# Performance work log

Hardware: AMD Instinct MI355X
Metric: run time of the kernel (lower is better)

The kernel has to match this reference:

```python
import jax, jax.numpy as jnp
import numpy as np

B, SQ, SKV, D = 4, 2048, 2048, 1024
HEADS, DIM_HEAD = 16, 64
SCALE = DIM_HEAD ** -0.5


def setup_inputs() -> dict:
    key = jax.random.key(0)
    ks = jax.random.split(key, 7)
    s = 0.02  # keep pre-softmax logits in a sane range
    return {
        "hidden_states": jax.random.normal(ks[0], (B, SQ, D), dtype=jnp.float32),
        "encoder_hidden_states": jax.random.normal(ks[1], (B, SKV, D), dtype=jnp.float32),
        "Wq": jax.random.normal(ks[2], (D, D), dtype=jnp.float32) * s,
        "Wk": jax.random.normal(ks[3], (D, D), dtype=jnp.float32) * s,
        "Wv": jax.random.normal(ks[4], (D, D), dtype=jnp.float32) * s,
        "Wo": jax.random.normal(ks[5], (D, D), dtype=jnp.float32) * s,
        "bo": jnp.zeros((D,), dtype=jnp.float32),
    }


def reference(hidden_states, encoder_hidden_states, Wq, Wk, Wv, Wo, bo):
    # to_q / to_k / to_v (bias=False)
    q = hidden_states @ Wq                       # [B, SQ, H*Dh]
    k = encoder_hidden_states @ Wk               # [B, SKV, H*Dh]
    v = encoder_hidden_states @ Wv
    # head split: [B, S, H, Dh]
    q = q.reshape(B, SQ, HEADS, DIM_HEAD)
    k = k.reshape(B, SKV, HEADS, DIM_HEAD)
    v = v.reshape(B, SKV, HEADS, DIM_HEAD)
    # scaled QK^T (baddbmm with beta=0, alpha=scale), softmax over keys
    scores = jnp.einsum("bqhd,bkhd->bhqk", q, k) * SCALE  # [B, H, SQ, SKV]
    probs = jax.nn.softmax(scores, axis=-1)
    # attention-weighted values, merge heads
    out = jnp.einsum("bhqk,bkhd->bqhd", probs, v).reshape(B, SQ, HEADS * DIM_HEAD)
    # to_out[0] linear (with bias); to_out[1] Dropout(0.0) is identity
    return out @ Wo + bo
```

## Files before the change

kernel.cpp:

```cpp
#include <hip/hip_runtime.h>

#define BATCH 4
#define SQ 2048
#define SKV 2048
#define DMODEL 1024
#define HEADS 16
#define DH 64

typedef __bf16 bf8_t __attribute__((ext_vector_type(8)));
typedef float f4_t __attribute__((ext_vector_type(4)));
typedef float f16_t __attribute__((ext_vector_type(16)));
typedef unsigned int u32;
typedef unsigned short ush;

static __device__ __forceinline__ ush f2bf(float f) {
  __bf16 h = (__bf16)f;
  return __builtin_bit_cast(ush, h);
}
static __device__ __forceinline__ u32 pk2(float a, float b) {
  return (u32)f2bf(a) | ((u32)f2bf(b) << 16);
}
static __device__ __forceinline__ void async16(const ush* g, ush* l) {
  __builtin_amdgcn_global_load_lds((const __attribute__((address_space(1))) unsigned int*)g,
                                   (__attribute__((address_space(3))) unsigned int*)l, 16, 0, 0);
}
static __device__ __forceinline__ void barrier_f() {
  asm volatile("" ::: "memory");
  __builtin_amdgcn_s_barrier();
  asm volatile("" ::: "memory");
}

__global__ __launch_bounds__(256) void prep_k(const float* __restrict__ hs,
                                              const float* __restrict__ ehs,
                                              const float* __restrict__ W0,
                                              const float* __restrict__ W1,
                                              const float* __restrict__ W2,
                                              const float* __restrict__ W3,
                                              ush* __restrict__ wT,
                                              ush* __restrict__ hsb, ush* __restrict__ ehsb) {
  __shared__ ush t[64][72];
  const int bx = blockIdx.x;
  const int tid = threadIdx.x;
  if (bx < 8192) {
    const float* X = bx < 4096 ? hs : ehs;
    ush* Y = bx < 4096 ? hsb : ehsb;
    const size_t i = ((size_t)(bx & 4095) * 256 + tid) * 8;
    float4 a = *reinterpret_cast<const float4*>(X + i);
    float4 b = *reinterpret_cast<const float4*>(X + i + 4);
    uint4 u = {pk2(a.x, a.y), pk2(a.z, a.w), pk2(b.x, b.y), pk2(b.z, b.w)};
    *reinterpret_cast<uint4*>(Y + i) = u;
    return;
  }
  const int idx = bx - 8192;
  const int z = idx >> 8, kb = (idx >> 4) & 15, nb = idx & 15;
  const float* W = z == 0 ? W0 : z == 1 ? W1 : z == 2 ? W2 : W3;
  const float scl = (z == 0) ? 0.125f * 1.44269504088896f : 1.0f;
  ush* o = wT + (size_t)z * (DMODEL * DMODEL);
  const int k0 = kb * 64, n0 = nb * 64;
#pragma unroll
  for (int it = 0; it < 4; ++it) {
    int c = tid + it * 256;
    int r = c >> 4, q4 = c & 15;
    float4 v = *reinterpret_cast<const float4*>(&W[(size_t)(k0 + r) * DMODEL + n0 + q4 * 4]);
    t[q4 * 4 + 0][r] = f2bf(v.x * scl);
    t[q4 * 4 + 1][r] = f2bf(v.y * scl);
    t[q4 * 4 + 2][r] = f2bf(v.z * scl);
    t[q4 * 4 + 3][r] = f2bf(v.w * scl);
  }
  __syncthreads();
#pragma unroll
  for (int it = 0; it < 2; ++it) {
    int c = tid + it * 256;
    int r = c >> 3, s8 = c & 7;
    uint4 pv;
    pv.x = (u32)t[r][s8 * 8 + 0] | ((u32)t[r][s8 * 8 + 1] << 16);
    pv.y = (u32)t[r][s8 * 8 + 2] | ((u32)t[r][s8 * 8 + 3] << 16);
    pv.z = (u32)t[r][s8 * 8 + 4] | ((u32)t[r][s8 * 8 + 5] << 16);
    pv.w = (u32)t[r][s8 * 8 + 6] | ((u32)t[r][s8 * 8 + 7] << 16);
    *reinterpret_cast<uint4*>(&o[(size_t)(n0 + r) * DMODEL + k0 + s8 * 8]) = pv;
  }
}

__global__ __launch_bounds__(256, 2) void proj_k(const ush* __restrict__ hsb,
                                                 const ush* __restrict__ ehsb,
                                                 const ush* __restrict__ AO,
                                                 const ush* __restrict__ wT,
                                                 ush* __restrict__ Qb, ush* __restrict__ K2,
                                                 ush* __restrict__ V2, float* __restrict__ out,
                                                 const float* __restrict__ bias, int segbase) {
  __shared__ ush As[2][128 * 64];
  __shared__ ush Bs[2][128 * 64];
  const int tid = threadIdx.x;
  const int lane = tid & 63, w = tid >> 6;
  const int wr = w >> 1, wc = w & 1;
  const int lr = lane & 15, lg = lane >> 4;
  const int bid = blockIdx.x;
  const int seg = segbase + (bid >> 9);
  const int t = bid & 511;
  const int m0 = (t >> 3) * 128, n0 = (t & 7) * 128;
  const ush* A = seg == 0 ? hsb : (seg == 3 ? AO : ehsb);
  const ush* BT = wT + (size_t)seg * (DMODEL * DMODEL);

  auto stage = [&](int bf, int kt) {
    const int kb = kt * 64;
#pragma unroll
    for (int ch = 0; ch < 4; ++ch) {
      const int g = ch * 256 + tid;
      const int r = g >> 3, s8 = (g & 7) ^ (r & 7);
      async16(A + (size_t)(m0 + r) * DMODEL + kb + s8 * 8, &As[bf][(ch * 256 + w * 64) * 8]);
      async16(BT + (size_t)(n0 + r) * DMODEL + kb + s8 * 8, &Bs[bf][(ch * 256 + w * 64) * 8]);
    }
  };

  f4_t acc[4][4] = {};
  stage(0, 0);
  for (int kt = 0; kt < DMODEL / 64; ++kt) {
    const int cur = kt & 1;
    barrier_f();
    if (kt + 1 < DMODEL / 64) {
      stage(cur ^ 1, kt + 1);
      asm volatile("s_waitcnt vmcnt(8)" ::: "memory");
    } else {
      asm volatile("s_waitcnt vmcnt(0)" ::: "memory");
    }
    barrier_f();
#pragma unroll
    for (int ks = 0; ks < 2; ++ks) {
      bf8_t a[4], b[4];
#pragma unroll
      for (int rf = 0; rf < 4; ++rf) {
        const int row = wr * 64 + rf * 16 + lr;
        a[rf] = *reinterpret_cast<const bf8_t*>(
            &As[cur][(row * 64 + ks * 32 + lg * 8) ^ ((row & 7) << 3)]);
      }
#pragma unroll
      for (int cf = 0; cf < 4; ++cf) {
        const int nn = wc * 64 + cf * 16 + lr;
        b[cf] = *reinterpret_cast<const bf8_t*>(
            &Bs[cur][(nn * 64 + ks * 32 + lg * 8) ^ ((nn & 7) << 3)]);
      }
      __builtin_amdgcn_s_setprio(1);
#pragma unroll
      for (int rf = 0; rf < 4; ++rf)
#pragma unroll
        for (int cf = 0; cf < 4; ++cf)
          acc[rf][cf] = __builtin_amdgcn_mfma_f32_16x16x32_bf16(a[rf], b[cf], acc[rf][cf], 0, 0, 0);
      __builtin_amdgcn_s_setprio(0);
    }
  }
  if (seg == 1 || seg == 2) {
    ush* L = &As[0][0];
    barrier_f();
#pragma unroll
    for (int rf = 0; rf < 4; ++rf)
#pragma unroll
      for (int cf = 0; cf < 4; ++cf) {
        const int nl = wc * 64 + cf * 16 + lr;
        const int h2 = nl >> 6, dd = nl & 63;
#pragma unroll
        for (int i = 0; i < 4; ++i) {
          const int kvl = wr * 64 + rf * 16 + lg * 4 + i;
          const int kt2 = kvl >> 6, s = kvl & 63;
          int idx;
          if (seg == 1) {
            idx = ((h2 * 2 + kt2) << 12) + (((dd >> 4) * 2 + ((dd >> 3) & 1)) << 9) +
                  (s << 3) + (dd & 7);
          } else {
            idx = ((h2 * 2 + kt2) << 12) + (((s >> 4) * 2 + ((s >> 3) & 1)) << 9) +
                  (dd << 3) + (s & 7);
          }
          L[idx] = f2bf(acc[rf][cf][i]);
        }
      }
    barrier_f();
    ush* G = (seg == 1) ? K2 : V2;
    const int bb = m0 >> 11, kt0 = (m0 & 2047) >> 6;
    const int h0 = n0 >> 6;
#pragma unroll
    for (int j = 0; j < 4; ++j) {
      const size_t dst =
          ((size_t)(bb * 16 + h0 + (j >> 1)) * 32 + kt0 + (j & 1)) * 4096 + tid * 16;
      *reinterpret_cast<uint4*>(&G[dst]) =
          *reinterpret_cast<const uint4*>(&L[j * 4096 + tid * 16]);
      *reinterpret_cast<uint4*>(&G[dst + 8]) =
          *reinterpret_cast<const uint4*>(&L[j * 4096 + tid * 16 + 8]);
    }
  } else if (seg == 3) {
#pragma unroll
    for (int cf = 0; cf < 4; ++cf) {
      const int col = n0 + wc * 64 + cf * 16 + lr;
      const float bv = bias[col];
#pragma unroll
      for (int rf = 0; rf < 4; ++rf)
#pragma unroll
        for (int i = 0; i < 4; ++i) {
          const int row = m0 + wr * 64 + rf * 16 + lg * 4 + i;
          out[(size_t)row * DMODEL + col] = acc[rf][cf][i] + bv;
        }
    }
  } else {
#pragma unroll
    for (int rf = 0; rf < 4; ++rf)
#pragma unroll
      for (int cf = 0; cf < 4; ++cf)
#pragma unroll
        for (int i = 0; i < 4; ++i) {
          const int row = m0 + wr * 64 + rf * 16 + lg * 4 + i;
          const int col = n0 + wc * 64 + cf * 16 + lr;
          Qb[(size_t)row * DMODEL + col] = f2bf(acc[rf][cf][i]);
        }
  }
}

__global__ __launch_bounds__(256, 4) void attn_k(const ush* __restrict__ Qb,
                                                 const ush* __restrict__ K2,
                                                 const ush* __restrict__ V2,
                                                 ush* __restrict__ AO) {
  __shared__ ush Ks[2][4096];
  __shared__ ush Vs[2][4096];
  const int tid = threadIdx.x;
  const int lane = tid & 63, w = tid >> 6;
  const int rw = lane & 31, hi = lane >> 5;

  const int bid = blockIdx.x;
  const int swz = (bid & 7) * 128 + (bid >> 3);
  const int hl = swz >> 4;
  const int qb = swz & 15;
  const int b = hl >> 4, h = hl & 15;
  const int q0 = qb * 128 + w * 32;

  const ush* Qp = Qb + ((size_t)(b * SQ + q0 + rw)) * DMODEL + h * DH + hi * 8;
  bf8_t qf[4];
#pragma unroll
  for (int f = 0; f < 4; ++f) qf[f] = *reinterpret_cast<const bf8_t*>(Qp + 16 * f);

  bf8_t ones;
#pragma unroll
  for (int i = 0; i < 8; ++i) ones[i] = __builtin_bit_cast(__bf16, (ush)0x3F80);

  f16_t acc0 = {}, acc1 = {}, sacc = {};

  const ush* Kh = K2 + (size_t)hl * 131072;
  const ush* Vh = V2 + (size_t)hl * 131072;

  auto stage = [&](int bf, int kt) {
    const ush* ksrc = Kh + (size_t)kt * 4096;
    const ush* vsrc = Vh + (size_t)kt * 4096;
#pragma unroll
    for (int ch = 0; ch < 2; ++ch) {
      const int off = (ch * 256 + tid) * 8;
      async16(ksrc + off, &Ks[bf][(ch * 256 + w * 64) * 8]);
      async16(vsrc + off, &Vs[bf][(ch * 256 + w * 64) * 8]);
    }
  };

  stage(0, 0);
  int cur = 0;
  for (int kt = 0; kt < SKV / 64; ++kt) {
    barrier_f();
    if (kt + 1 < SKV / 64) {
      stage(cur ^ 1, kt + 1);
      asm volatile("s_waitcnt vmcnt(4)" ::: "memory");
    } else {
      asm volatile("s_waitcnt vmcnt(0)" ::: "memory");
    }
    barrier_f();

    f16_t s0 = {}, s1 = {};
    __builtin_amdgcn_s_setprio(1);
#pragma unroll
    for (int f = 0; f < 4; ++f) {
      const int base = (f * 128 + hi * 64 + rw) * 8;
      bf8_t k0 = *reinterpret_cast<const bf8_t*>(&Ks[cur][base]);
      bf8_t k1 = *reinterpret_cast<const bf8_t*>(&Ks[cur][base + 256]);
      s0 = __builtin_amdgcn_mfma_f32_32x32x16_bf16(k0, qf[f], s0, 0, 0, 0);
      s1 = __builtin_amdgcn_mfma_f32_32x32x16_bf16(k1, qf[f], s1, 0, 0, 0);
    }
    __builtin_amdgcn_s_setprio(0);

#pragma unroll
    for (int i = 0; i < 16; ++i) s0[i] = __builtin_amdgcn_exp2f(s0[i]);
#pragma unroll
    for (int i = 0; i < 16; ++i) s1[i] = __builtin_amdgcn_exp2f(s1[i]);

    __builtin_amdgcn_s_setprio(1);
#pragma unroll
    for (int kb = 0; kb < 2; ++kb) {
      const f16_t& sv = kb ? s1 : s0;
      bf8_t pf[2];
      {
        u32 w0 = pk2(sv[0], sv[1]), w2 = pk2(sv[4], sv[5]);
        asm volatile("v_permlane32_swap_b32 %0, %1" : "+v"(w0), "+v"(w2));
        u32 w1 = pk2(sv[2], sv[3]), w3 = pk2(sv[6], sv[7]);
        asm volatile("v_permlane32_swap_b32 %0, %1" : "+v"(w1), "+v"(w3));
        uint4 t0 = {w0, w1, w2, w3};
        pf[0] = __builtin_bit_cast(bf8_t, t0);
        u32 x0 = pk2(sv[8], sv[9]), x2 = pk2(sv[12], sv[13]);
        asm volatile("v_permlane32_swap_b32 %0, %1" : "+v"(x0), "+v"(x2));
        u32 x1 = pk2(sv[10], sv[11]), x3 = pk2(sv[14], sv[15]);
        asm volatile("v_permlane32_swap_b32 %0, %1" : "+v"(x1), "+v"(x3));
        uint4 t1 = {x0, x1, x2, x3};
        pf[1] = __builtin_bit_cast(bf8_t, t1);
      }
#pragma unroll
      for (int s = 0; s < 2; ++s) {
        const int vbase = ((2 * kb + s) * 128 + hi * 64 + rw) * 8;
        bf8_t v0 = *reinterpret_cast<const bf8_t*>(&Vs[cur][vbase]);
        bf8_t v1 = *reinterpret_cast<const bf8_t*>(&Vs[cur][vbase + 256]);
        acc0 = __builtin_amdgcn_mfma_f32_32x32x16_bf16(v0, pf[s], acc0, 0, 0, 0);
        acc1 = __builtin_amdgcn_mfma_f32_32x32x16_bf16(v1, pf[s], acc1, 0, 0, 0);
        sacc = __builtin_amdgcn_mfma_f32_32x32x16_bf16(ones, pf[s], sacc, 0, 0, 0);
      }
    }
    __builtin_amdgcn_s_setprio(0);
    cur ^= 1;
  }

  const float inv = 1.f / sacc[0];
  ush* Op = AO + ((size_t)(b * SQ + q0 + rw)) * DMODEL + h * DH;
#pragma unroll
  for (int db = 0; db < 2; ++db) {
    const f16_t& A = db ? acc1 : acc0;
#pragma unroll
    for (int r = 0; r < 16; r += 2) {
      const int d = db * 32 + (r & 3) + 8 * (r >> 2) + 4 * hi;
      *reinterpret_cast<u32*>(Op + d) = pk2(A[r] * inv, A[r + 1] * inv);
    }
  }
}

extern "C" void kernel_launch(void* const* d_in, const int* in_sizes, int n_in,
                              void* d_out, int out_size, void* d_ws, size_t ws_size,
                              hipStream_t stream) {
  const float* hs = (const float*)d_in[0];
  const float* ehs = (const float*)d_in[1];
  const float* Wq = (const float*)d_in[2];
  const float* Wk = (const float*)d_in[3];
  const float* Wv = (const float*)d_in[4];
  const float* Wo = (const float*)d_in[5];
  const float* bo = (const float*)d_in[6];
  float* out = (float*)d_out;

  unsigned short* ws = (unsigned short*)d_ws;
  const size_t MM = (size_t)1024 * 1024;
  unsigned short* wT = ws;
  unsigned short* Qb = ws + 4 * MM;
  unsigned short* K2 = Qb + 8 * MM;
  unsigned short* V2 = K2 + 8 * MM;
  unsigned short* AO = V2 + 8 * MM;
  unsigned short* hsb = (unsigned short*)d_out;
  unsigned short* ehsb = hsb + 8 * MM;

  prep_k<<<dim3(9216), 256, 0, stream>>>(hs, ehs, Wq, Wk, Wv, Wo, wT, hsb, ehsb);
  proj_k<<<dim3(1536), 256, 0, stream>>>(hsb, ehsb, AO, wT, Qb, K2, V2, out, bo, 0);
  attn_k<<<dim3(1024), 256, 0, stream>>>(Qb, K2, V2, AO);
  proj_k<<<dim3(512), 256, 0, stream>>>(hsb, ehsb, AO, wT, Qb, K2, V2, out, bo, 3);
}
```

Baseline: 207.3 us.

## Load K/V fragments directly from global memory and sum probabilities with VALU

The attention kernel drops the LDS double-buffered K/V staging and its barriers; each wave now loads its K and V MFMA fragments straight from global memory into registers every tile. The row-sum of exponentials is computed with VALU adds plus a cross-half shuffle instead of an extra MFMA against a ones vector. Occupancy hint drops from 4 to 3 blocks per CU because of higher register use. The cost is that every wave in a block re-reads the same K/V tiles from global/L2 instead of sharing them through LDS, and load latency is no longer hidden by explicit prefetch.

```diff
diff --git a/kernel.cpp b/kernel.cpp
--- a/kernel.cpp
+++ b/kernel.cpp
@@ -212,12 +212,10 @@
   }
 }
 
-__global__ __launch_bounds__(256, 4) void attn_k(const ush* __restrict__ Qb,
+__global__ __launch_bounds__(256, 3) void attn_k(const ush* __restrict__ Qb,
                                                  const ush* __restrict__ K2,
                                                  const ush* __restrict__ V2,
                                                  ush* __restrict__ AO) {
-  __shared__ ush Ks[2][4096];
-  __shared__ ush Vs[2][4096];
   const int tid = threadIdx.x;
   const int lane = tid & 63, w = tid >> 6;
   const int rw = lane & 31, hi = lane >> 5;
@@ -234,47 +232,36 @@
 #pragma unroll
   for (int f = 0; f < 4; ++f) qf[f] = *reinterpret_cast<const bf8_t*>(Qp + 16 * f);
 
-  bf8_t ones;
-#pragma unroll
-  for (int i = 0; i < 8; ++i) ones[i] = __builtin_bit_cast(__bf16, (ush)0x3F80);
-
-  f16_t acc0 = {}, acc1 = {}, sacc = {};
-
-  const ush* Kh = K2 + (size_t)hl * 131072;
-  const ush* Vh = V2 + (size_t)hl * 131072;
-
-  auto stage = [&](int bf, int kt) {
-    const ush* ksrc = Kh + (size_t)kt * 4096;
-    const ush* vsrc = Vh + (size_t)kt * 4096;
-#pragma unroll
-    for (int ch = 0; ch < 2; ++ch) {
-      const int off = (ch * 256 + tid) * 8;
-      async16(ksrc + off, &Ks[bf][(ch * 256 + w * 64) * 8]);
-      async16(vsrc + off, &Vs[bf][(ch * 256 + w * 64) * 8]);
-    }
-  };
-
-  stage(0, 0);
-  int cur = 0;
+  f16_t acc0 = {}, acc1 = {};
+  float lsum = 0.f;
+
+  const int fo = (hi * 64 + rw) * 8;
+  const ush* Kh = K2 + (size_t)hl * 131072 + fo;
+  const ush* Vh = V2 + (size_t)hl * 131072 + fo;
+
   for (int kt = 0; kt < SKV / 64; ++kt) {
-    barrier_f();
-    if (kt + 1 < SKV / 64) {
-      stage(cur ^ 1, kt + 1);
-      asm volatile("s_waitcnt vmcnt(4)" ::: "memory");
-    } else {
-      asm volatile("s_waitcnt vmcnt(0)" ::: "memory");
-    }
-    barrier_f();
+    const ush* kp = Kh + kt * 4096;
+    const ush* vp = Vh + kt * 4096;
+
+    bf8_t kf0[4], kf1[4];
+#pragma unroll
+    for (int f = 0; f < 4; ++f) {
+      kf0[f] = *reinterpret_cast<const bf8_t*>(kp + f * 1024);
+      kf1[f] = *reinterpret_cast<const bf8_t*>(kp + f * 1024 + 256);
+    }
+    bf8_t vf0[4], vf1[4];
+#pragma unroll
+    for (int g = 0; g < 4; ++g) {
+      vf0[g] = *reinterpret_cast<const bf8_t*>(vp + g * 1024);
+      vf1[g] = *reinterpret_cast<const bf8_t*>(vp + g * 1024 + 256);
+    }
 
     f16_t s0 = {}, s1 = {};
     __builtin_amdgcn_s_setprio(1);
 #pragma unroll
     for (int f = 0; f < 4; ++f) {
-      const int base = (f * 128 + hi * 64 + rw) * 8;
-      bf8_t k0 = *reinterpret_cast<const bf8_t*>(&Ks[cur][base]);
-      bf8_t k1 = *reinterpret_cast<const bf8_t*>(&Ks[cur][base + 256]);
-      s0 = __builtin_amdgcn_mfma_f32_32x32x16_bf16(k0, qf[f], s0, 0, 0, 0);
-      s1 = __builtin_amdgcn_mfma_f32_32x32x16_bf16(k1, qf[f], s1, 0, 0, 0);
+      s0 = __builtin_amdgcn_mfma_f32_32x32x16_bf16(kf0[f], qf[f], s0, 0, 0, 0);
+      s1 = __builtin_amdgcn_mfma_f32_32x32x16_bf16(kf1[f], qf[f], s1, 0, 0, 0);
     }
     __builtin_amdgcn_s_setprio(0);
 
@@ -282,6 +269,21 @@
     for (int i = 0; i < 16; ++i) s0[i] = __builtin_amdgcn_exp2f(s0[i]);
 #pragma unroll
     for (int i = 0; i < 16; ++i) s1[i] = __builtin_amdgcn_exp2f(s1[i]);
+    {
+      float t0 = 0.f, t1 = 0.f, t2 = 0.f, t3 = 0.f;
+#pragma unroll
+      for (int i = 0; i < 16; i += 4) {
+        t0 += s0[i];
+        t1 += s0[i + 1];
+        t2 += s0[i + 2];
+        t3 += s0[i + 3];
+        t0 += s1[i];
+        t1 += s1[i + 1];
+        t2 += s1[i + 2];
+        t3 += s1[i + 3];
+      }
+      lsum += (t0 + t1) + (t2 + t3);
+    }
 
     __builtin_amdgcn_s_setprio(1);
 #pragma unroll
@@ -304,19 +306,16 @@
       }
 #pragma unroll
       for (int s = 0; s < 2; ++s) {
-        const int vbase = ((2 * kb + s) * 128 + hi * 64 + rw) * 8;
-        bf8_t v0 = *reinterpret_cast<const bf8_t*>(&Vs[cur][vbase]);
-        bf8_t v1 = *reinterpret_cast<const bf8_t*>(&Vs[cur][vbase + 256]);
-        acc0 = __builtin_amdgcn_mfma_f32_32x32x16_bf16(v0, pf[s], acc0, 0, 0, 0);
-        acc1 = __builtin_amdgcn_mfma_f32_32x32x16_bf16(v1, pf[s], acc1, 0, 0, 0);
-        sacc = __builtin_amdgcn_mfma_f32_32x32x16_bf16(ones, pf[s], sacc, 0, 0, 0);
+        const int g = 2 * kb + s;
+        acc0 = __builtin_amdgcn_mfma_f32_32x32x16_bf16(vf0[g], pf[s], acc0, 0, 0, 0);
+        acc1 = __builtin_amdgcn_mfma_f32_32x32x16_bf16(vf1[g], pf[s], acc1, 0, 0, 0);
       }
     }
     __builtin_amdgcn_s_setprio(0);
-    cur ^= 1;
-  }
-
-  const float inv = 1.f / sacc[0];
+  }
+
+  const float lrow = lsum + __shfl_xor(lsum, 32, 64);
+  const float inv = 1.f / lrow;
   ush* Op = AO + ((size_t)(b * SQ + q0 + rw)) * DMODEL + h * DH;
 #pragma unroll
   for (int db = 0; db < 2; ++db) {
```

New measurement: 206.6 us. About the same (-0.3%).
